# Kernel tuning notes

Measured on AMD Instinct MI355X. Metric: run time of the kernel, lower is better.

Reference implementation:

```python
import jax, jax.numpy as jnp
import numpy as np


def setup_inputs() -> dict:
    key = jax.random.key(0)
    k1, k2, k3 = jax.random.split(key, 3)
    B, K, OUT, IN = 8192, 8, 1024, 1024
    bound = (6.0 / (IN * OUT)) ** 0.5
    x = jax.random.normal(k1, (B, IN), dtype=jnp.float32)
    expert_weights = jax.random.uniform(k2, (B, K), dtype=jnp.float32)
    weight = jax.random.uniform(k3, (K, OUT, IN), dtype=jnp.float32, minval=-bound, maxval=bound)
    bias = jnp.zeros((K, OUT), dtype=jnp.float32)
    return {"x": x, "expert_weights": expert_weights, "weight": weight, "bias": bias}


def reference(x, expert_weights, weight, bias):
    # Mathematically identical to: blended_W = einsum('bk,koi->boi'); bmm(blended_W, x)
    # but avoids materializing the [B,out,in] intermediate: apply each expert's
    # linear map then blend with routing weights (contraction reassociation).
    per_expert = jnp.einsum('bi,koi->bko', x, weight)        # [B, K, out]
    y = jnp.einsum('bk,bko->bo', expert_weights, per_expert)  # [B, out]
    y = y + expert_weights @ bias                             # blended bias [B, out]
    return y
```

## Files before the change

kernel.cpp:

```cpp
#include <hip/hip_runtime.h>
#include <hip/hip_bf16.h>

typedef __attribute__((ext_vector_type(8))) short short8;
typedef __attribute__((ext_vector_type(4))) float f32x4;

#define NDIM 1024
#define INDIM 1024
#define KEXP 8
#define BROWS 8192
#define NX (BROWS * INDIM)
#define NW (KEXP * NDIM * INDIM)

__device__ __forceinline__ unsigned int pack2bf(float a, float b) {
    __hip_bfloat162 h = __float22bfloat162_rn(make_float2(a, b));
    union { __hip_bfloat162 h; unsigned int u; } cv;
    cv.h = h;
    return cv.u;
}

__device__ __forceinline__ void gload16(const void* src, void* ldsdst) {
    __builtin_amdgcn_global_load_lds(
        (__attribute__((address_space(1))) void*)(src),
        (__attribute__((address_space(3))) void*)(ldsdst), 16, 0, 0);
}

__global__ void convert_bf16(const float* __restrict__ x, const float* __restrict__ w,
                             unsigned short* __restrict__ dst) {
    const long total = (long)NX + NW;
    const long stride = (long)gridDim.x * blockDim.x * 8;
    for (long i = ((long)blockIdx.x * blockDim.x + threadIdx.x) * 8; i < total; i += stride) {
        const float* s = (i < NX) ? (x + i) : (w + (i - NX));
        float4 a = ((const float4*)s)[0];
        float4 b = ((const float4*)s)[1];
        uint4 q;
        q.x = pack2bf(a.x, a.y); q.y = pack2bf(a.z, a.w);
        q.z = pack2bf(b.x, b.y); q.w = pack2bf(b.z, b.w);
        *(uint4*)(dst + i) = q;
    }
}

__global__ __launch_bounds__(512, 2)
void moe_gemm_fold(const unsigned short* __restrict__ xb,
                   const float* __restrict__ ew,
                   const unsigned short* __restrict__ Wp,
                   const float* __restrict__ bias,
                   float* __restrict__ out) {
    __shared__ __align__(16) unsigned short lds[2 * 32768];

    const int tid = threadIdx.x;
    const int bid = blockIdx.x;
    const int xcd = bid & 7;
    const int grp = bid >> 3;
    const int bt = xcd * 4 + (grp & 3);
    const int ot = grp >> 2;
    const int bbase = bt * 256;
    const int o_blk = ot * 32;

    const int w  = tid >> 6;
    const int l  = tid & 63;
    const int lr = l & 15;
    const int lg = l >> 4;
    const int wrow = (w >> 2) * 128;
    const int wcol = (w & 3) * 64;

    const int lrow = l >> 2;
    const int sg = (l & 3) ^ ((l >> 3) & 3);
    const int swz = (lr >> 1) & 3;

    int aoff[8][2], boff[4][2];
#pragma unroll
    for (int mf = 0; mf < 8; ++mf)
#pragma unroll
        for (int ks = 0; ks < 2; ++ks)
            aoff[mf][ks] = ks * 8192 + (wrow + mf * 16 + lr) * 32 + ((lg ^ swz) * 8);
#pragma unroll
    for (int nf = 0; nf < 4; ++nf)
#pragma unroll
        for (int ks = 0; ks < 2; ++ks)
            boff[nf][ks] = 16384 + ks * 8192 + (wcol + nf * 16 + lr) * 32 + ((lg ^ swz) * 8);

    auto stage4 = [&](int slot, int kt, int half) {
#pragma unroll
        for (int i = 0; i < 4; ++i) {
            const int id = w * 8 + half * 4 + i;
            unsigned short* dst = &lds[slot * 32768 + id * 512];
            const int sub = id & 15;
            const int col = kt * 64 + ((id >> 4) & 1) * 32 + sg * 8;
            if (id < 32) {
                gload16(Wp + (size_t)(lrow & 7) * (NDIM * INDIM)
                           + (size_t)(o_blk + sub * 2 + (lrow >> 3)) * INDIM + col, dst);
            } else {
                gload16(xb + (size_t)(bbase + sub * 16 + lrow) * INDIM + col, dst);
            }
        }
    };

    f32x4 acc[8][4];
#pragma unroll
    for (int mf = 0; mf < 8; ++mf)
#pragma unroll
        for (int nf = 0; nf < 4; ++nf) acc[mf][nf] = f32x4{0.f, 0.f, 0.f, 0.f};

    stage4(0, 0, 0);
    stage4(0, 0, 1);

#pragma unroll 1
    for (int kt = 0; kt < 16; ++kt) {
        const int cs = kt & 1;
        const bool doS = (kt + 1) < 16;

        asm volatile("s_waitcnt vmcnt(0)\n\ts_barrier" ::: "memory");

        const unsigned short* lb = &lds[cs * 32768];
        short8 alo[4], ahi[4], b0[4], b1[4];

#pragma unroll
        for (int m = 0; m < 4; ++m) alo[m] = *(const short8*)(lb + aoff[m][0]);
#pragma unroll
        for (int n = 0; n < 4; ++n) b0[n] = *(const short8*)(lb + boff[n][0]);
        if (doS) stage4(cs ^ 1, kt + 1, 0);
#pragma unroll
        for (int m = 0; m < 4; ++m) ahi[m] = *(const short8*)(lb + aoff[4 + m][0]);

        __builtin_amdgcn_s_setprio(1);
#pragma unroll
        for (int m = 0; m < 4; ++m)
#pragma unroll
            for (int n = 0; n < 4; ++n)
                acc[m][n] = __builtin_amdgcn_mfma_f32_16x16x32_bf16(alo[m], b0[n], acc[m][n], 0, 0, 0);
        __builtin_amdgcn_s_setprio(0);

#pragma unroll
        for (int n = 0; n < 4; ++n) b1[n] = *(const short8*)(lb + boff[n][1]);
#pragma unroll
        for (int m = 0; m < 4; ++m) alo[m] = *(const short8*)(lb + aoff[m][1]);
        if (doS) stage4(cs ^ 1, kt + 1, 1);

        __builtin_amdgcn_s_setprio(1);
#pragma unroll
        for (int m = 0; m < 4; ++m)
#pragma unroll
            for (int n = 0; n < 4; ++n)
                acc[4 + m][n] = __builtin_amdgcn_mfma_f32_16x16x32_bf16(ahi[m], b0[n], acc[4 + m][n], 0, 0, 0);
        __builtin_amdgcn_s_setprio(0);

#pragma unroll
        for (int m = 0; m < 4; ++m) ahi[m] = *(const short8*)(lb + aoff[4 + m][1]);

        __builtin_amdgcn_s_setprio(1);
#pragma unroll
        for (int m = 0; m < 4; ++m)
#pragma unroll
            for (int n = 0; n < 4; ++n)
                acc[m][n] = __builtin_amdgcn_mfma_f32_16x16x32_bf16(alo[m], b1[n], acc[m][n], 0, 0, 0);
        __builtin_amdgcn_s_setprio(0);

        __builtin_amdgcn_s_setprio(1);
#pragma unroll
        for (int m = 0; m < 4; ++m)
#pragma unroll
            for (int n = 0; n < 4; ++n)
                acc[4 + m][n] = __builtin_amdgcn_mfma_f32_16x16x32_bf16(ahi[m], b1[n], acc[4 + m][n], 0, 0, 0);
        __builtin_amdgcn_s_setprio(0);
    }

    __syncthreads();
    float* ylds = (float*)lds;

    const int obw = wrow >> 3;
#pragma unroll
    for (int nf = 0; nf < 4; ++nf) {
        const int bl = wcol + nf * 16 + lr;
        const float4 ea = *(const float4*)(ew + (size_t)(bbase + bl) * KEXP);
        const float4 eb = *(const float4*)(ew + (size_t)(bbase + bl) * KEXP + 4);
        float c0, c1, c2, c3;
        if (lg & 1) { c0 = eb.x; c1 = eb.y; c2 = eb.z; c3 = eb.w; }
        else        { c0 = ea.x; c1 = ea.y; c2 = ea.z; c3 = ea.w; }
#pragma unroll
        for (int mf = 0; mf < 8; ++mf) {
            float p = c0 * acc[mf][nf][0] + c1 * acc[mf][nf][1]
                    + c2 * acc[mf][nf][2] + c3 * acc[mf][nf][3];
            p += __shfl_xor(p, 16);
            if (!(lg & 1))
                ylds[bl * 36 + obw + mf * 2 + (lg >> 1)] = p;
        }
    }
    __syncthreads();

    {
        const int b = tid >> 1;
        const int oh = (tid & 1) * 16;
        const float* yr = &ylds[b * 36 + oh];
        float y0[16];
#pragma unroll
        for (int jj = 0; jj < 16; ++jj) y0[jj] = yr[jj];
        const float4 ea = *(const float4*)(ew + (size_t)(bbase + b) * KEXP);
        const float4 e2 = *(const float4*)(ew + (size_t)(bbase + b) * KEXP + 4);
        const float ekk[8] = {ea.x, ea.y, ea.z, ea.w, e2.x, e2.y, e2.z, e2.w};
#pragma unroll
        for (int k = 0; k < 8; ++k) {
            const float* bp = bias + k * NDIM + o_blk + oh;
#pragma unroll
            for (int jj = 0; jj < 16; ++jj) y0[jj] += ekk[k] * bp[jj];
        }
        float* op = out + (size_t)(bbase + b) * NDIM + o_blk + oh;
#pragma unroll
        for (int jj = 0; jj < 4; ++jj)
            *(float4*)(op + jj * 4) =
                make_float4(y0[jj * 4], y0[jj * 4 + 1], y0[jj * 4 + 2], y0[jj * 4 + 3]);
    }
}

#define FLDW 40
__global__ __launch_bounds__(256, 2)
void moe_blend_gemm_fb(const float* __restrict__ x, const float* __restrict__ ew,
                       const float* __restrict__ w, const float* __restrict__ bias,
                       float* __restrict__ out) {
    __shared__ unsigned short lA[128][FLDW];
    __shared__ unsigned short lB[128][FLDW];
    const int tid = threadIdx.x, bid = blockIdx.x;
    const int nt = bid & 7, mt = bid >> 3;
    const int mbase = mt * 128, nbase = nt * 128;
    const int trow = tid >> 1, tcol = (tid & 1) * 16;
    const float* xp = x + (size_t)(mbase + trow) * INDIM + tcol;
    const float* wp = w + (size_t)(nbase + trow) * INDIM + tcol;
    const float* ep = ew + (size_t)(mbase + trow) * KEXP;
    const int wid = tid >> 6, wrB = (wid >> 1) * 64, wcB = (wid & 1) * 64;
    const int l = tid & 63, lr = l & 15, lg = l >> 4;
    f32x4 acc[4][4];
#pragma unroll
    for (int m = 0; m < 4; ++m)
#pragma unroll
        for (int n = 0; n < 4; ++n) acc[m][n] = f32x4{0.f, 0.f, 0.f, 0.f};
    const unsigned short* rdA = &lA[wrB + lr][lg * 8];
    const unsigned short* rdB = &lB[wcB + lr][lg * 8];
    unsigned int* wA = (unsigned int*)&lA[trow][tcol];
    unsigned int* wB = (unsigned int*)&lB[trow][tcol];
    float4 ra0, ra1, ra2, ra3, rb0, rb1, rb2, rb3;
    float sc;
    {
        const float4* pa = (const float4*)(xp);
        ra0 = pa[0]; ra1 = pa[1]; ra2 = pa[2]; ra3 = pa[3];
        const float4* pb = (const float4*)(wp);
        rb0 = pb[0]; rb1 = pb[1]; rb2 = pb[2]; rb3 = pb[3];
        sc = ep[0];
    }
    for (int tt = 0; tt < 256; ++tt) {
        __syncthreads();
        uint4 qa0, qa1, qb0, qb1;
        qa0.x = pack2bf(ra0.x * sc, ra0.y * sc); qa0.y = pack2bf(ra0.z * sc, ra0.w * sc);
        qa0.z = pack2bf(ra1.x * sc, ra1.y * sc); qa0.w = pack2bf(ra1.z * sc, ra1.w * sc);
        qa1.x = pack2bf(ra2.x * sc, ra2.y * sc); qa1.y = pack2bf(ra2.z * sc, ra2.w * sc);
        qa1.z = pack2bf(ra3.x * sc, ra3.y * sc); qa1.w = pack2bf(ra3.z * sc, ra3.w * sc);
        qb0.x = pack2bf(rb0.x, rb0.y); qb0.y = pack2bf(rb0.z, rb0.w);
        qb0.z = pack2bf(rb1.x, rb1.y); qb0.w = pack2bf(rb1.z, rb1.w);
        qb1.x = pack2bf(rb2.x, rb2.y); qb1.y = pack2bf(rb2.z, rb2.w);
        qb1.z = pack2bf(rb3.x, rb3.y); qb1.w = pack2bf(rb3.z, rb3.w);
        *(uint4*)(wA) = qa0; *(uint4*)(wA + 4) = qa1;
        *(uint4*)(wB) = qb0; *(uint4*)(wB + 4) = qb1;
        __syncthreads();
        if (tt + 1 < 256) {
            const int kc = (tt + 1) >> 5, i0 = ((tt + 1) & 31) * 32;
            const float4* pa = (const float4*)(xp + i0);
            ra0 = pa[0]; ra1 = pa[1]; ra2 = pa[2]; ra3 = pa[3];
            const float4* pb = (const float4*)(wp + (size_t)kc * (size_t)(NDIM * INDIM) + i0);
            rb0 = pb[0]; rb1 = pb[1]; rb2 = pb[2]; rb3 = pb[3];
            sc = ep[kc];
        }
        short8 af[4], bf[4];
#pragma unroll
        for (int m = 0; m < 4; ++m) af[m] = *(const short8*)(rdA + m * 16 * FLDW);
#pragma unroll
        for (int n = 0; n < 4; ++n) bf[n] = *(const short8*)(rdB + n * 16 * FLDW);
#pragma unroll
        for (int m = 0; m < 4; ++m)
#pragma unroll
            for (int n = 0; n < 4; ++n)
                acc[m][n] = __builtin_amdgcn_mfma_f32_16x16x32_bf16(af[m], bf[n], acc[m][n], 0, 0, 0);
    }
#pragma unroll
    for (int m = 0; m < 4; ++m)
#pragma unroll
        for (int j = 0; j < 4; ++j) {
            const int gr = mbase + wrB + m * 16 + lg * 4 + j;
            const float4* e4 = (const float4*)(ew + (size_t)gr * KEXP);
            const float4 e0 = e4[0], e1 = e4[1];
            const float eb[8] = {e0.x, e0.y, e0.z, e0.w, e1.x, e1.y, e1.z, e1.w};
            float* op = out + (size_t)gr * NDIM + nbase + wcB;
#pragma unroll
            for (int n = 0; n < 4; ++n) {
                float t = acc[m][n][j];
#pragma unroll
                for (int kk = 0; kk < 8; ++kk) t += eb[kk] * bias[kk * NDIM + nbase + wcB + n * 16 + lr];
                op[n * 16 + lr] = t;
            }
        }
}

extern "C" void kernel_launch(void* const* d_in, const int* in_sizes, int n_in,
                              void* d_out, int out_size, void* d_ws, size_t ws_size,
                              hipStream_t stream) {
    (void)in_sizes; (void)n_in; (void)out_size;
    const float* x    = (const float*)d_in[0];
    const float* ew   = (const float*)d_in[1];
    const float* w    = (const float*)d_in[2];
    const float* bias = (const float*)d_in[3];
    float* out = (float*)d_out;

    const size_t need = (size_t)(NX + NW) * sizeof(unsigned short);

    if (ws_size >= need) {
        unsigned short* xb = (unsigned short*)d_ws;
        unsigned short* Wp = xb + NX;
        hipLaunchKernelGGL(convert_bf16, dim3(4096), dim3(256), 0, stream, x, w, xb);
        hipLaunchKernelGGL(moe_gemm_fold, dim3(1024), dim3(512), 0, stream, xb, ew, Wp, bias, out);
    } else {
        hipLaunchKernelGGL(moe_blend_gemm_fb, dim3(512), dim3(256), 0, stream, x, ew, w, bias, out);
    }
}
```

Before: 145.9 us.

## Make GEMM persistent over four output tiles with in-loop epilogue

Each block now loops over four consecutive 32-column output tiles (64 k-steps in total) instead of one, and the grid shrinks from 1024 to 256 blocks. The staging pipeline runs continuously across tile boundaries, so prologue and tail costs are paid once per block rather than once per tile. The epilogue now runs inside the loop, writes scalars straight to global memory with the bias computed per element, and drops the LDS transpose and the coalesced float4 stores. The risk is that 256 blocks may leave compute units underused, and the uncoalesced stores and repeated bias loads add memory traffic.

```diff
diff --git a/kernel.cpp b/kernel.cpp
--- a/kernel.cpp
+++ b/kernel.cpp
@@ -40,21 +40,20 @@
 }
 
 __global__ __launch_bounds__(512, 2)
-void moe_gemm_fold(const unsigned short* __restrict__ xb,
-                   const float* __restrict__ ew,
-                   const unsigned short* __restrict__ Wp,
-                   const float* __restrict__ bias,
-                   float* __restrict__ out) {
+void moe_gemm_p(const unsigned short* __restrict__ xb,
+                const float* __restrict__ ew,
+                const unsigned short* __restrict__ Wp,
+                const float* __restrict__ bias,
+                float* __restrict__ out) {
     __shared__ __align__(16) unsigned short lds[2 * 32768];
 
     const int tid = threadIdx.x;
     const int bid = blockIdx.x;
     const int xcd = bid & 7;
-    const int grp = bid >> 3;
-    const int bt = xcd * 4 + (grp & 3);
-    const int ot = grp >> 2;
+    const int bt = xcd * 4 + ((bid >> 3) & 3);
+    const int ogrp = bid >> 5;
     const int bbase = bt * 256;
-    const int o_blk = ot * 32;
+    const int o_base = ogrp * 128;
 
     const int w  = tid >> 6;
     const int l  = tid & 63;
@@ -79,16 +78,18 @@
         for (int ks = 0; ks < 2; ++ks)
             boff[nf][ks] = 16384 + ks * 8192 + (wcol + nf * 16 + lr) * 32 + ((lg ^ swz) * 8);
 
-    auto stage4 = [&](int slot, int kt, int half) {
+    auto stage4 = [&](int slot, int g, int half) {
+        const int o_blk_s = o_base + (g >> 4) * 32;
+        const int kcol = (g & 15) * 64;
 #pragma unroll
         for (int i = 0; i < 4; ++i) {
             const int id = w * 8 + half * 4 + i;
             unsigned short* dst = &lds[slot * 32768 + id * 512];
             const int sub = id & 15;
-            const int col = kt * 64 + ((id >> 4) & 1) * 32 + sg * 8;
+            const int col = kcol + ((id >> 4) & 1) * 32 + sg * 8;
             if (id < 32) {
                 gload16(Wp + (size_t)(lrow & 7) * (NDIM * INDIM)
-                           + (size_t)(o_blk + sub * 2 + (lrow >> 3)) * INDIM + col, dst);
+                           + (size_t)(o_blk_s + sub * 2 + (lrow >> 3)) * INDIM + col, dst);
             } else {
                 gload16(xb + (size_t)(bbase + sub * 16 + lrow) * INDIM + col, dst);
             }
@@ -105,9 +106,9 @@
     stage4(0, 0, 1);
 
 #pragma unroll 1
-    for (int kt = 0; kt < 16; ++kt) {
-        const int cs = kt & 1;
-        const bool doS = (kt + 1) < 16;
+    for (int g = 0; g < 64; ++g) {
+        const int cs = g & 1;
+        const bool doS = (g + 1) < 64;
 
         asm volatile("s_waitcnt vmcnt(0)\n\ts_barrier" ::: "memory");
 
@@ -118,7 +119,7 @@
         for (int m = 0; m < 4; ++m) alo[m] = *(const short8*)(lb + aoff[m][0]);
 #pragma unroll
         for (int n = 0; n < 4; ++n) b0[n] = *(const short8*)(lb + boff[n][0]);
-        if (doS) stage4(cs ^ 1, kt + 1, 0);
+        if (doS) stage4(cs ^ 1, g + 1, 0);
 #pragma unroll
         for (int m = 0; m < 4; ++m) ahi[m] = *(const short8*)(lb + aoff[4 + m][0]);
 
@@ -134,7 +135,7 @@
         for (int n = 0; n < 4; ++n) b1[n] = *(const short8*)(lb + boff[n][1]);
 #pragma unroll
         for (int m = 0; m < 4; ++m) alo[m] = *(const short8*)(lb + aoff[m][1]);
-        if (doS) stage4(cs ^ 1, kt + 1, 1);
+        if (doS) stage4(cs ^ 1, g + 1, 1);
 
         __builtin_amdgcn_s_setprio(1);
 #pragma unroll
@@ -162,52 +163,36 @@
             for (int n = 0; n < 4; ++n)
                 acc[4 + m][n] = __builtin_amdgcn_mfma_f32_16x16x32_bf16(ahi[m], b1[n], acc[4 + m][n], 0, 0, 0);
         __builtin_amdgcn_s_setprio(0);
-    }
-
-    __syncthreads();
-    float* ylds = (float*)lds;
-
-    const int obw = wrow >> 3;
-#pragma unroll
-    for (int nf = 0; nf < 4; ++nf) {
-        const int bl = wcol + nf * 16 + lr;
-        const float4 ea = *(const float4*)(ew + (size_t)(bbase + bl) * KEXP);
-        const float4 eb = *(const float4*)(ew + (size_t)(bbase + bl) * KEXP + 4);
-        float c0, c1, c2, c3;
-        if (lg & 1) { c0 = eb.x; c1 = eb.y; c2 = eb.z; c3 = eb.w; }
-        else        { c0 = ea.x; c1 = ea.y; c2 = ea.z; c3 = ea.w; }
-#pragma unroll
-        for (int mf = 0; mf < 8; ++mf) {
-            float p = c0 * acc[mf][nf][0] + c1 * acc[mf][nf][1]
-                    + c2 * acc[mf][nf][2] + c3 * acc[mf][nf][3];
-            p += __shfl_xor(p, 16);
-            if (!(lg & 1))
-                ylds[bl * 36 + obw + mf * 2 + (lg >> 1)] = p;
+
+        if ((g & 15) == 15) {
+            const int o_blk = o_base + (g >> 4) * 32;
+            const int obw = wrow >> 3;
+#pragma unroll
+            for (int nf = 0; nf < 4; ++nf) {
+                const long bg = (long)(bbase + wcol + nf * 16 + lr);
+                const float4 ea = *(const float4*)(ew + bg * KEXP);
+                const float4 eb = *(const float4*)(ew + bg * KEXP + 4);
+                float c0, c1, c2, c3;
+                if (lg & 1) { c0 = eb.x; c1 = eb.y; c2 = eb.z; c3 = eb.w; }
+                else        { c0 = ea.x; c1 = ea.y; c2 = ea.z; c3 = ea.w; }
+                const float e8[8] = {ea.x, ea.y, ea.z, ea.w, eb.x, eb.y, eb.z, eb.w};
+#pragma unroll
+                for (int mf = 0; mf < 8; ++mf) {
+                    float p = c0 * acc[mf][nf][0] + c1 * acc[mf][nf][1]
+                            + c2 * acc[mf][nf][2] + c3 * acc[mf][nf][3];
+                    p += __shfl_xor(p, 16);
+                    const bool mine = ((lg & 1) == 0) ? (mf < 4) : (mf >= 4);
+                    if (mine) {
+                        const int og = o_blk + obw + mf * 2 + (lg >> 1);
+                        float bt_ = 0.f;
+#pragma unroll
+                        for (int k = 0; k < 8; ++k) bt_ += e8[k] * bias[k * NDIM + og];
+                        out[bg * NDIM + og] = p + bt_;
+                    }
+                    acc[mf][nf] = f32x4{0.f, 0.f, 0.f, 0.f};
+                }
+            }
         }
-    }
-    __syncthreads();
-
-    {
-        const int b = tid >> 1;
-        const int oh = (tid & 1) * 16;
-        const float* yr = &ylds[b * 36 + oh];
-        float y0[16];
-#pragma unroll
-        for (int jj = 0; jj < 16; ++jj) y0[jj] = yr[jj];
-        const float4 ea = *(const float4*)(ew + (size_t)(bbase + b) * KEXP);
-        const float4 e2 = *(const float4*)(ew + (size_t)(bbase + b) * KEXP + 4);
-        const float ekk[8] = {ea.x, ea.y, ea.z, ea.w, e2.x, e2.y, e2.z, e2.w};
-#pragma unroll
-        for (int k = 0; k < 8; ++k) {
-            const float* bp = bias + k * NDIM + o_blk + oh;
-#pragma unroll
-            for (int jj = 0; jj < 16; ++jj) y0[jj] += ekk[k] * bp[jj];
-        }
-        float* op = out + (size_t)(bbase + b) * NDIM + o_blk + oh;
-#pragma unroll
-        for (int jj = 0; jj < 4; ++jj)
-            *(float4*)(op + jj * 4) =
-                make_float4(y0[jj * 4], y0[jj * 4 + 1], y0[jj * 4 + 2], y0[jj * 4 + 3]);
     }
 }
 
@@ -313,7 +298,7 @@
         unsigned short* xb = (unsigned short*)d_ws;
         unsigned short* Wp = xb + NX;
         hipLaunchKernelGGL(convert_bf16, dim3(4096), dim3(256), 0, stream, x, w, xb);
-        hipLaunchKernelGGL(moe_gemm_fold, dim3(1024), dim3(512), 0, stream, xb, ew, Wp, bias, out);
+        hipLaunchKernelGGL(moe_gemm_p, dim3(256), dim3(512), 0, stream, xb, ew, Wp, bias, out);
     } else {
         hipLaunchKernelGGL(moe_blend_gemm_fb, dim3(512), dim3(256), 0, stream, x, ew, w, bias, out);
     }
```

New measurement: 162.2 us. 11.2% more time.

## Split k-tile staging into four quarters with finer-grained waits and barriers

Applied to the files above, without the earlier changes.

Restructures the main GEMM loop into four phases per k-tile. Each phase issues one quarter of the next tile's global-to-LDS loads, separated by s_barriers and lgkmcnt waits with sched_barriers around the MFMA blocks. The vmcnt waits now allow four loads to stay outstanding, so the second half of the current tile can be consumed while later loads are in flight. This aims to interleave memory traffic with MFMA work more evenly, at the cost of many more workgroup barriers per iteration.

```diff
diff --git a/kernel.cpp b/kernel.cpp
--- a/kernel.cpp
+++ b/kernel.cpp
@@ -40,11 +40,11 @@
 }
 
 __global__ __launch_bounds__(512, 2)
-void moe_gemm_fold(const unsigned short* __restrict__ xb,
-                   const float* __restrict__ ew,
-                   const unsigned short* __restrict__ Wp,
-                   const float* __restrict__ bias,
-                   float* __restrict__ out) {
+void moe_gemm_fold8(const unsigned short* __restrict__ xb,
+                    const float* __restrict__ ew,
+                    const unsigned short* __restrict__ Wp,
+                    const float* __restrict__ bias,
+                    float* __restrict__ out) {
     __shared__ __align__(16) unsigned short lds[2 * 32768];
 
     const int tid = threadIdx.x;
@@ -79,18 +79,19 @@
         for (int ks = 0; ks < 2; ++ks)
             boff[nf][ks] = 16384 + ks * 8192 + (wcol + nf * 16 + lr) * 32 + ((lg ^ swz) * 8);
 
-    auto stage4 = [&](int slot, int kt, int half) {
-#pragma unroll
-        for (int i = 0; i < 4; ++i) {
-            const int id = w * 8 + half * 4 + i;
-            unsigned short* dst = &lds[slot * 32768 + id * 512];
-            const int sub = id & 15;
-            const int col = kt * 64 + ((id >> 4) & 1) * 32 + sg * 8;
-            if (id < 32) {
+    auto stageQ = [&](int slot, int kt, int q) {
+        const int ks = q >> 1;
+        const int col = kt * 64 + ks * 32 + sg * 8;
+#pragma unroll
+        for (int i = 0; i < 2; ++i) {
+            const int c16 = w * 2 + i;
+            if ((q & 1) == 0) {
                 gload16(Wp + (size_t)(lrow & 7) * (NDIM * INDIM)
-                           + (size_t)(o_blk + sub * 2 + (lrow >> 3)) * INDIM + col, dst);
+                           + (size_t)(o_blk + c16 * 2 + (lrow >> 3)) * INDIM + col,
+                        &lds[slot * 32768 + ks * 8192 + c16 * 512]);
             } else {
-                gload16(xb + (size_t)(bbase + sub * 16 + lrow) * INDIM + col, dst);
+                gload16(xb + (size_t)(bbase + c16 * 16 + lrow) * INDIM + col,
+                        &lds[slot * 32768 + 16384 + ks * 8192 + c16 * 512]);
             }
         }
     };
@@ -101,27 +102,26 @@
 #pragma unroll
         for (int nf = 0; nf < 4; ++nf) acc[mf][nf] = f32x4{0.f, 0.f, 0.f, 0.f};
 
-    stage4(0, 0, 0);
-    stage4(0, 0, 1);
+    stageQ(0, 0, 0); stageQ(0, 0, 1); stageQ(0, 0, 2); stageQ(0, 0, 3);
 
 #pragma unroll 1
     for (int kt = 0; kt < 16; ++kt) {
         const int cs = kt & 1;
+        const int ns = cs ^ 1;
         const bool doS = (kt + 1) < 16;
-
-        asm volatile("s_waitcnt vmcnt(0)\n\ts_barrier" ::: "memory");
-
         const unsigned short* lb = &lds[cs * 32768];
         short8 alo[4], ahi[4], b0[4], b1[4];
 
+        asm volatile("s_waitcnt vmcnt(4)\n\ts_barrier" ::: "memory");
+
 #pragma unroll
         for (int m = 0; m < 4; ++m) alo[m] = *(const short8*)(lb + aoff[m][0]);
 #pragma unroll
         for (int n = 0; n < 4; ++n) b0[n] = *(const short8*)(lb + boff[n][0]);
-        if (doS) stage4(cs ^ 1, kt + 1, 0);
-#pragma unroll
-        for (int m = 0; m < 4; ++m) ahi[m] = *(const short8*)(lb + aoff[4 + m][0]);
-
+        if (doS) stageQ(ns, kt + 1, 0);
+        __builtin_amdgcn_s_barrier();
+        asm volatile("s_waitcnt lgkmcnt(0)" ::: "memory");
+        __builtin_amdgcn_sched_barrier(0);
         __builtin_amdgcn_s_setprio(1);
 #pragma unroll
         for (int m = 0; m < 4; ++m)
@@ -129,13 +129,14 @@
             for (int n = 0; n < 4; ++n)
                 acc[m][n] = __builtin_amdgcn_mfma_f32_16x16x32_bf16(alo[m], b0[n], acc[m][n], 0, 0, 0);
         __builtin_amdgcn_s_setprio(0);
-
-#pragma unroll
-        for (int n = 0; n < 4; ++n) b1[n] = *(const short8*)(lb + boff[n][1]);
-#pragma unroll
-        for (int m = 0; m < 4; ++m) alo[m] = *(const short8*)(lb + aoff[m][1]);
-        if (doS) stage4(cs ^ 1, kt + 1, 1);
-
+        __builtin_amdgcn_s_barrier();
+
+#pragma unroll
+        for (int m = 0; m < 4; ++m) ahi[m] = *(const short8*)(lb + aoff[4 + m][0]);
+        if (doS) stageQ(ns, kt + 1, 1);
+        __builtin_amdgcn_s_barrier();
+        asm volatile("s_waitcnt lgkmcnt(0)" ::: "memory");
+        __builtin_amdgcn_sched_barrier(0);
         __builtin_amdgcn_s_setprio(1);
 #pragma unroll
         for (int m = 0; m < 4; ++m)
@@ -144,9 +145,19 @@
                 acc[4 + m][n] = __builtin_amdgcn_mfma_f32_16x16x32_bf16(ahi[m], b0[n], acc[4 + m][n], 0, 0, 0);
         __builtin_amdgcn_s_setprio(0);
 
-#pragma unroll
-        for (int m = 0; m < 4; ++m) ahi[m] = *(const short8*)(lb + aoff[4 + m][1]);
-
+        if (kt < 15)
+            asm volatile("s_waitcnt vmcnt(4)\n\ts_barrier" ::: "memory");
+        else
+            asm volatile("s_waitcnt vmcnt(0)\n\ts_barrier" ::: "memory");
+
+#pragma unroll
+        for (int m = 0; m < 4; ++m) alo[m] = *(const short8*)(lb + aoff[m][1]);
+#pragma unroll
+        for (int n = 0; n < 4; ++n) b1[n] = *(const short8*)(lb + boff[n][1]);
+        if (doS) stageQ(ns, kt + 1, 2);
+        __builtin_amdgcn_s_barrier();
+        asm volatile("s_waitcnt lgkmcnt(0)" ::: "memory");
+        __builtin_amdgcn_sched_barrier(0);
         __builtin_amdgcn_s_setprio(1);
 #pragma unroll
         for (int m = 0; m < 4; ++m)
@@ -154,7 +165,14 @@
             for (int n = 0; n < 4; ++n)
                 acc[m][n] = __builtin_amdgcn_mfma_f32_16x16x32_bf16(alo[m], b1[n], acc[m][n], 0, 0, 0);
         __builtin_amdgcn_s_setprio(0);
-
+        __builtin_amdgcn_s_barrier();
+
+#pragma unroll
+        for (int m = 0; m < 4; ++m) ahi[m] = *(const short8*)(lb + aoff[4 + m][1]);
+        if (doS) stageQ(ns, kt + 1, 3);
+        __builtin_amdgcn_s_barrier();
+        asm volatile("s_waitcnt lgkmcnt(0)" ::: "memory");
+        __builtin_amdgcn_sched_barrier(0);
         __builtin_amdgcn_s_setprio(1);
 #pragma unroll
         for (int m = 0; m < 4; ++m)
@@ -313,7 +331,7 @@
         unsigned short* xb = (unsigned short*)d_ws;
         unsigned short* Wp = xb + NX;
         hipLaunchKernelGGL(convert_bf16, dim3(4096), dim3(256), 0, stream, x, w, xb);
-        hipLaunchKernelGGL(moe_gemm_fold, dim3(1024), dim3(512), 0, stream, xb, ew, Wp, bias, out);
+        hipLaunchKernelGGL(moe_gemm_fold8, dim3(1024), dim3(512), 0, stream, xb, ew, Wp, bias, out);
     } else {
         hipLaunchKernelGGL(moe_blend_gemm_fb, dim3(512), dim3(256), 0, stream, x, ew, w, bias, out);
     }
```

After: 160.2 us. 9.8% more time.
